# Kernel optimization log

Measured on AMD Instinct MI355X. Metric: run time of the kernel, lower is better.

The kernel has to match this reference:

```python
import jax, jax.numpy as jnp
import numpy as np


def _gcn_conv(x, W, b, src, dst, deg_inv_sqrt, n_nodes):
    # x: [N, Fin], W: [Fin, Fout]; edges (with self-loops): src, dst [E+N]
    h = x @ W  # [N, Fout]
    norm = deg_inv_sqrt[src] * deg_inv_sqrt[dst]  # [E+N]
    msgs = h[src] * norm[:, None]  # gather-multiply
    out = jax.ops.segment_sum(msgs, dst, num_segments=n_nodes)  # scatter-add
    return out + b


def setup_inputs() -> dict:
    key = jax.random.key(0)
    k1, k2, k3, k4 = jax.random.split(key, 4)
    N, E, FIN, HID, OUT = 100000, 3200000, 128, 32, 32
    x = jax.random.normal(k1, (N, FIN), dtype=jnp.float32)
    edge_index = jax.random.randint(k2, (2, E), 0, N, dtype=jnp.int64)
    W1 = jax.random.normal(k3, (FIN, HID), dtype=jnp.float32) * (1.0 / np.sqrt(FIN))
    b1 = jnp.zeros((HID,), dtype=jnp.float32)
    W2 = jax.random.normal(k4, (HID, OUT), dtype=jnp.float32) * (1.0 / np.sqrt(HID))
    b2 = jnp.zeros((OUT,), dtype=jnp.float32)
    return {"x": x, "edge_index": edge_index, "W1": W1, "b1": b1, "W2": W2, "b2": b2}


def reference(x, edge_index, W1, b1, W2, b2):
    n = x.shape[0]
    # GCNConv defaults: add self-loops, symmetric normalization D^-1/2 (A+I) D^-1/2
    loops = jnp.arange(n, dtype=edge_index.dtype)
    src = jnp.concatenate([edge_index[0], loops])
    dst = jnp.concatenate([edge_index[1], loops])
    deg = jax.ops.segment_sum(jnp.ones_like(dst, dtype=x.dtype), dst, num_segments=n)
    deg_inv_sqrt = jnp.where(deg > 0, jax.lax.rsqrt(jnp.maximum(deg, 1.0)), 0.0)
    h = jax.nn.relu(_gcn_conv(x, W1, b1, src, dst, deg_inv_sqrt, n))  # hidden layer + ReLU
    out = jax.nn.relu(_gcn_conv(h, W2, b2, src, dst, deg_inv_sqrt, n))  # last layer + last_activation relu
    return out
```

## Files before the change

### kernel.cpp

```cpp
#include <hip/hip_runtime.h>
#include <hip/hip_fp16.h>

#define FIN 128
#define HID 32
#define BSHIFT 8
#define BNODES 256
#define CHUNK 2048
#define NBMAX 512
#define CAPB 8960
#define G1ROWS 64
#define XPAD 4


__global__ __launch_bounds__(256) void chunk_sort_kernel(const int* __restrict__ src,
                                                         const int* __restrict__ dst,
                                                         int* __restrict__ ec,
                                                         unsigned short* __restrict__ offt,
                                                         int E, int nb) {
    __shared__ int hist[NBMAX];
    __shared__ int pref[NBMAX];
    __shared__ int sorted[CHUNK];
    int c = blockIdx.x, t = threadIdx.x;
    int beg = c * CHUNK;
    int cnt = min(CHUNK, E - beg);
    for (int i = t; i < nb; i += 256) hist[i] = 0;
    __syncthreads();
    int bk[8], ent[8];
    #pragma unroll
    for (int j = 0; j < 8; ++j) {
        int i = t + j * 256;
        if (i < cnt) {
            int d = dst[beg + i];
            bk[j]  = ((unsigned)d) >> BSHIFT;
            ent[j] = src[beg + i] | ((d & (BNODES - 1)) << 24);
            atomicAdd(&hist[bk[j]], 1);
        } else bk[j] = -1;
    }
    __syncthreads();
    if (t < 64) {
        int v[8];
        int s = 0;
        #pragma unroll
        for (int j = 0; j < 8; ++j) {
            int idx = t * 8 + j;
            int h = (idx < nb) ? hist[idx] : 0;
            v[j] = s; s += h;
        }
        int run = s;
        #pragma unroll
        for (int d = 1; d < 64; d <<= 1) {
            int o = __shfl_up(run, d, 64);
            if (t >= d) run += o;
        }
        int excl = run - s;
        #pragma unroll
        for (int j = 0; j < 8; ++j) {
            int idx = t * 8 + j;
            if (idx < nb) { int p = excl + v[j]; pref[idx] = p; hist[idx] = p; }
        }
    }
    __syncthreads();
    #pragma unroll
    for (int j = 0; j < 8; ++j) {
        if (bk[j] >= 0) {
            int p = atomicAdd(&hist[bk[j]], 1);
            sorted[p] = ent[j];
        }
    }
    __syncthreads();
    for (int i = t; i < cnt; i += 256) ec[(size_t)c * CHUNK + i] = sorted[i];
    unsigned short* row = offt + (size_t)c * (nb + 1);
    for (int i = t; i < nb; i += 256) row[i] = (unsigned short)pref[i];
    if (t == 0) row[nb] = (unsigned short)cnt;
}


__global__ __launch_bounds__(1024) void bucket_build_kernel(const int* __restrict__ ec,
                                                            const unsigned short* __restrict__ offt,
                                                            int* __restrict__ entries,
                                                            float* __restrict__ dinv,
                                                            int* __restrict__ rowbeg,
                                                            int* __restrict__ rowcnt,
                                                            int n, int nb, int nchunks, int cap) {
    __shared__ int raw[CAPB];
    __shared__ int srt[CAPB];
    __shared__ int hist[BNODES];
    __shared__ int pref[BNODES];
    __shared__ int cursor[BNODES];
    __shared__ int nfill;
    int b = blockIdx.x, t = threadIdx.x;
    if (t < BNODES) hist[t] = 0;
    if (t == 0) nfill = 0;
    __syncthreads();
    for (int c = t; c < nchunks; c += 1024) {
        const unsigned short* row = offt + (size_t)c * (nb + 1);
        int s = row[b], e2 = row[b + 1];
        int m = e2 - s;
        if (m > 0) {
            int base = atomicAdd(&nfill, m);
            const int* p = ec + (size_t)c * CHUNK + s;
            int k = 0;
            for (; k + 4 <= m; k += 4) {
                int e0 = p[k], e1 = p[k + 1], e2v = p[k + 2], e3 = p[k + 3];
                if (base + k + 0 < CAPB) raw[base + k + 0] = e0;
                if (base + k + 1 < CAPB) raw[base + k + 1] = e1;
                if (base + k + 2 < CAPB) raw[base + k + 2] = e2v;
                if (base + k + 3 < CAPB) raw[base + k + 3] = e3;
                atomicAdd(&hist[((unsigned)e0) >> 24], 1);
                atomicAdd(&hist[((unsigned)e1) >> 24], 1);
                atomicAdd(&hist[((unsigned)e2v) >> 24], 1);
                atomicAdd(&hist[((unsigned)e3) >> 24], 1);
            }
            for (; k < m; ++k) {
                int e = p[k];
                if (base + k < CAPB) raw[base + k] = e;
                atomicAdd(&hist[((unsigned)e) >> 24], 1);
            }
        }
    }
    __syncthreads();
    int total = min(nfill, CAPB);
    if (t < 64) {
        int v[4];
        int s = 0;
        #pragma unroll
        for (int j = 0; j < 4; ++j) { v[j] = s; s += hist[t * 4 + j]; }
        int run = s;
        #pragma unroll
        for (int d = 1; d < 64; d <<= 1) {
            int o = __shfl_up(run, d, 64);
            if (t >= d) run += o;
        }
        int excl = run - s;
        #pragma unroll
        for (int j = 0; j < 4; ++j) {
            int idx = t * 4 + j;
            int p = excl + v[j];
            pref[idx] = p; cursor[idx] = p;
        }
    }
    __syncthreads();
    for (int i = t; i < total; i += 1024) {
        int e = raw[i];
        int p = atomicAdd(&cursor[((unsigned)e) >> 24], 1);
        srt[p] = e;
    }
    __syncthreads();
    int* ep = entries + (size_t)b * cap;
    for (int i = t; i < total; i += 1024) ep[i] = srt[i];
    int node = b * BNODES + t;
    if (t < BNODES && node < n) {
        int deg = hist[t];
        dinv[node]   = rsqrtf((float)deg + 1.0f);
        rowbeg[node] = b * cap + pref[t];
        rowcnt[node] = deg;
    }
}


__global__ __launch_bounds__(256) void gemm1_kernel(const float* __restrict__ x,
                                                    const float* __restrict__ W,
                                                    const float* __restrict__ dinv,
                                                    __half* __restrict__ h16, int n) {
    __shared__ float Ws[FIN * HID];
    int t = threadIdx.x;
    for (int i = t; i < FIN * HID; i += 256) Ws[i] = W[i];
    __syncthreads();
    int row0 = blockIdx.x * G1ROWS;
    int tr = t >> 3, tc = t & 7;
    int r0 = row0 + tr * 2, c0 = tc * 4;
    bool v0 = r0 < n, v1 = (r0 + 1) < n;
    const float* p0 = v0 ? &x[(size_t)r0 * FIN] : x;
    const float* p1 = v1 ? &x[(size_t)(r0 + 1) * FIN] : x;
    float4 a0 = make_float4(0.f, 0.f, 0.f, 0.f);
    float4 a1 = make_float4(0.f, 0.f, 0.f, 0.f);
    #pragma unroll 8
    for (int k4 = 0; k4 < FIN / 4; ++k4) {
        float4 xv0 = *(const float4*)&p0[k4 * 4];
        float4 xv1 = *(const float4*)&p1[k4 * 4];
        float4 w0 = *(const float4*)&Ws[(k4 * 4 + 0) * HID + c0];
        float4 w1 = *(const float4*)&Ws[(k4 * 4 + 1) * HID + c0];
        float4 w2 = *(const float4*)&Ws[(k4 * 4 + 2) * HID + c0];
        float4 w3 = *(const float4*)&Ws[(k4 * 4 + 3) * HID + c0];
        a0.x = fmaf(xv0.x, w0.x, a0.x); a0.y = fmaf(xv0.x, w0.y, a0.y);
        a0.z = fmaf(xv0.x, w0.z, a0.z); a0.w = fmaf(xv0.x, w0.w, a0.w);
        a0.x = fmaf(xv0.y, w1.x, a0.x); a0.y = fmaf(xv0.y, w1.y, a0.y);
        a0.z = fmaf(xv0.y, w1.z, a0.z); a0.w = fmaf(xv0.y, w1.w, a0.w);
        a0.x = fmaf(xv0.z, w2.x, a0.x); a0.y = fmaf(xv0.z, w2.y, a0.y);
        a0.z = fmaf(xv0.z, w2.z, a0.z); a0.w = fmaf(xv0.z, w2.w, a0.w);
        a0.x = fmaf(xv0.w, w3.x, a0.x); a0.y = fmaf(xv0.w, w3.y, a0.y);
        a0.z = fmaf(xv0.w, w3.z, a0.z); a0.w = fmaf(xv0.w, w3.w, a0.w);
        a1.x = fmaf(xv1.x, w0.x, a1.x); a1.y = fmaf(xv1.x, w0.y, a1.y);
        a1.z = fmaf(xv1.x, w0.z, a1.z); a1.w = fmaf(xv1.x, w0.w, a1.w);
        a1.x = fmaf(xv1.y, w1.x, a1.x); a1.y = fmaf(xv1.y, w1.y, a1.y);
        a1.z = fmaf(xv1.y, w1.z, a1.z); a1.w = fmaf(xv1.y, w1.w, a1.w);
        a1.x = fmaf(xv1.z, w2.x, a1.x); a1.y = fmaf(xv1.z, w2.y, a1.y);
        a1.z = fmaf(xv1.z, w2.z, a1.z); a1.w = fmaf(xv1.z, w2.w, a1.w);
        a1.x = fmaf(xv1.w, w3.x, a1.x); a1.y = fmaf(xv1.w, w3.y, a1.y);
        a1.z = fmaf(xv1.w, w3.z, a1.z); a1.w = fmaf(xv1.w, w3.w, a1.w);
    }
    #pragma unroll
    for (int rr = 0; rr < 2; ++rr) {
        int row = r0 + rr;
        float4 a = rr ? a1 : a0;
        float sc = (row < n) ? dinv[row] : 0.f;
        __half2 q0 = __floats2half2_rn(a.x * sc, a.y * sc);
        __half2 q1 = __floats2half2_rn(a.z * sc, a.w * sc);
        __half2* dstp = (__half2*)&h16[(size_t)row * HID + c0];
        dstp[0] = q0;
        dstp[1] = q1;
    }
}


template <int FUSEW2>
__global__ __launch_bounds__(256) void gather_kernel(const int* __restrict__ entries,
                                                     const int* __restrict__ rowbeg,
                                                     const int* __restrict__ rowcnt,
                                                     const float* __restrict__ dinv,
                                                     const __half* __restrict__ h16,
                                                     const float* __restrict__ bias,
                                                     const float* __restrict__ W2,
                                                     __half* __restrict__ houth,
                                                     float* __restrict__ outf,
                                                     int n, int sent) {
    __shared__ float Ws[HID * HID];
    int t = threadIdx.x;
    if (FUSEW2) {
        for (int i = t; i < HID * HID; i += 256) Ws[i] = W2[i];
        __syncthreads();
    }
    int g = t >> 2, f = t & 3;
    int i = blockIdx.x * 64 + g;
    if (i >= n) return;
    float di = dinv[i];
    float a[8];
    {
        float4 sv4 = *(const float4*)&h16[(size_t)i * HID + f * 8];
        const __half2* sh = (const __half2*)&sv4;
        #pragma unroll
        for (int q = 0; q < 4; ++q) {
            float2 fp = __half22float2(sh[q]);
            a[2 * q] = fp.x; a[2 * q + 1] = fp.y;
        }
    }
    int beg = rowbeg[i], cnt = rowcnt[i];
    for (int base = 0; base < cnt; base += 8) {
        int i0 = base + f, i1 = base + 4 + f;
        int sv0 = (i0 < cnt) ? entries[beg + i0] : sent;
        int sv1 = (i1 < cnt) ? entries[beg + i1] : sent;
        sv0 &= 0xFFFFFF; sv1 &= 0xFFFFFF;
        float4 hv[8];
        #pragma unroll
        for (int j = 0; j < 4; ++j) {
            int e = __shfl(sv0, j, 4);
            hv[j] = *(const float4*)&h16[(size_t)e * HID + f * 8];
        }
        #pragma unroll
        for (int j = 0; j < 4; ++j) {
            int e = __shfl(sv1, j, 4);
            hv[4 + j] = *(const float4*)&h16[(size_t)e * HID + f * 8];
        }
        #pragma unroll
        for (int j = 0; j < 8; ++j) {
            const __half2* hp = (const __half2*)&hv[j];
            #pragma unroll
            for (int q = 0; q < 4; ++q) {
                float2 fp = __half22float2(hp[q]);
                a[2 * q] += fp.x; a[2 * q + 1] += fp.y;
            }
        }
    }
    float4 b0 = *(const float4*)&bias[f * 8];
    float4 b1 = *(const float4*)&bias[f * 8 + 4];
    float bj[8] = {b0.x, b0.y, b0.z, b0.w, b1.x, b1.y, b1.z, b1.w};
    float rl[8];
    #pragma unroll
    for (int j = 0; j < 8; ++j) rl[j] = fmaxf(bj[j] + di * a[j], 0.f);

    if (!FUSEW2) {
        *(float4*)&outf[(size_t)i * HID + f * 8]     = make_float4(rl[0], rl[1], rl[2], rl[3]);
        *(float4*)&outf[(size_t)i * HID + f * 8 + 4] = make_float4(rl[4], rl[5], rl[6], rl[7]);
    } else {
        int c0 = f * 8;
        float o[8] = {0.f, 0.f, 0.f, 0.f, 0.f, 0.f, 0.f, 0.f};
        #pragma unroll
        for (int s = 0; s < 4; ++s) {
            #pragma unroll
            for (int j = 0; j < 8; ++j) {
                float av = __shfl(rl[j], s, 4);
                int k = s * 8 + j;
                float4 w0 = *(const float4*)&Ws[k * HID + c0];
                float4 w1 = *(const float4*)&Ws[k * HID + c0 + 4];
                o[0] = fmaf(av, w0.x, o[0]); o[1] = fmaf(av, w0.y, o[1]);
                o[2] = fmaf(av, w0.z, o[2]); o[3] = fmaf(av, w0.w, o[3]);
                o[4] = fmaf(av, w1.x, o[4]); o[5] = fmaf(av, w1.y, o[5]);
                o[6] = fmaf(av, w1.z, o[6]); o[7] = fmaf(av, w1.w, o[7]);
            }
        }
        float4 tmp;
        __half2* hp2 = (__half2*)&tmp;
        #pragma unroll
        for (int j = 0; j < 4; ++j) hp2[j] = __floats2half2_rn(di * o[2 * j], di * o[2 * j + 1]);
        *(float4*)&houth[(size_t)i * HID + f * 8] = tmp;
    }
}

extern "C" void kernel_launch(void* const* d_in, const int* in_sizes, int n_in,
                              void* d_out, int out_size, void* d_ws, size_t ws_size,
                              hipStream_t stream) {
    const float* x  = (const float*)d_in[0];
    const int*   ei = (const int*)d_in[1];
    const float* W1 = (const float*)d_in[2];
    const float* b1 = (const float*)d_in[3];
    const float* W2 = (const float*)d_in[4];
    const float* b2 = (const float*)d_in[5];
    float* out = (float*)d_out;

    int n = in_sizes[0] / FIN;
    int E = in_sizes[1] / 2;
    const int* src = ei;
    const int* dst = ei + E;

    int nb = (n + BNODES - 1) / BNODES;
    int nchunks = (E + CHUNK - 1) / CHUNK;
    int ggrid = (n + G1ROWS) / G1ROWS;
    int npad = ggrid * G1ROWS;
    int cap = CAPB;

    char* ws = (char*)d_ws;
    size_t off = 0;
    auto alloc = [&](size_t bytes) { char* p = ws + off; off += (bytes + 255) & ~(size_t)255; return p; };
    int*            ec      = (int*)alloc((size_t)nchunks * CHUNK * 4);
    unsigned short* offt    = (unsigned short*)alloc((size_t)nchunks * (nb + 1) * 2);
    int*            entries = (int*)alloc((size_t)nb * cap * 4);
    float*          dinv    = (float*)alloc((size_t)n * 4);
    int*            rowbeg  = (int*)alloc((size_t)n * 4);
    int*            rowcnt  = (int*)alloc((size_t)n * 4);
    __half*         hha     = (__half*)alloc((size_t)npad * HID * 2);
    __half*         hhb     = (__half*)alloc((size_t)(n + 1) * HID * 2);

    hipMemsetAsync(hhb + (size_t)n * HID, 0, HID * 2, stream);

    chunk_sort_kernel<<<nchunks, 256, 0, stream>>>(src, dst, ec, offt, E, nb);
    bucket_build_kernel<<<nb, 1024, 0, stream>>>(ec, offt, entries, dinv, rowbeg, rowcnt,
                                                 n, nb, nchunks, cap);

    gemm1_kernel<<<ggrid, 256, 0, stream>>>(x, W1, dinv, hha, n);
    gather_kernel<1><<<(n + 63) / 64, 256, 0, stream>>>(entries, rowbeg, rowcnt, dinv, hha,
                                                        b1, W2, hhb, nullptr, n, n);

    gather_kernel<0><<<(n + 63) / 64, 256, 0, stream>>>(entries, rowbeg, rowcnt, dinv, hhb,
                                                        b2, nullptr, nullptr, out, n, n);
}
```

Measured before the change: 242.6 us.

## Transpose chunk offset table, lane-split bucket copy, drop shared sort buffer

Chunks grow to 4096 edges with 512-thread blocks, and the per-chunk bucket offset table is stored transposed so each bucket's offsets sit contiguously across chunks, making bucket_build's offset reads coalesced. Bucket build now uses 512 threads with four lanes per chunk cooperatively copying entries, which replaces serial per-thread loops. The scatter into sorted order writes straight to global memory instead of staging through a second shared array, cutting shared memory and a sync. The costs are strided scattered writes of the transposed offsets in chunk_sort and uncoalesced global scatter writes in bucket build.

```diff
diff --git a/kernel.cpp b/kernel.cpp
--- a/kernel.cpp
+++ b/kernel.cpp
@@ -5,30 +5,29 @@
 #define HID 32
 #define BSHIFT 8
 #define BNODES 256
-#define CHUNK 2048
+#define CHUNK 4096
 #define NBMAX 512
 #define CAPB 8960
 #define G1ROWS 64
-#define XPAD 4
-
-
-__global__ __launch_bounds__(256) void chunk_sort_kernel(const int* __restrict__ src,
+
+
+__global__ __launch_bounds__(512) void chunk_sort_kernel(const int* __restrict__ src,
                                                          const int* __restrict__ dst,
                                                          int* __restrict__ ec,
-                                                         unsigned short* __restrict__ offt,
-                                                         int E, int nb) {
+                                                         unsigned short* __restrict__ offtT,
+                                                         int E, int nb, int nchunks) {
     __shared__ int hist[NBMAX];
     __shared__ int pref[NBMAX];
     __shared__ int sorted[CHUNK];
     int c = blockIdx.x, t = threadIdx.x;
     int beg = c * CHUNK;
     int cnt = min(CHUNK, E - beg);
-    for (int i = t; i < nb; i += 256) hist[i] = 0;
+    for (int i = t; i < nb; i += 512) hist[i] = 0;
     __syncthreads();
     int bk[8], ent[8];
     #pragma unroll
     for (int j = 0; j < 8; ++j) {
-        int i = t + j * 256;
+        int i = t + j * 512;
         if (i < cnt) {
             int d = dst[beg + i];
             bk[j]  = ((unsigned)d) >> BSHIFT;
@@ -68,22 +67,20 @@
         }
     }
     __syncthreads();
-    for (int i = t; i < cnt; i += 256) ec[(size_t)c * CHUNK + i] = sorted[i];
-    unsigned short* row = offt + (size_t)c * (nb + 1);
-    for (int i = t; i < nb; i += 256) row[i] = (unsigned short)pref[i];
-    if (t == 0) row[nb] = (unsigned short)cnt;
-}
-
-
-__global__ __launch_bounds__(1024) void bucket_build_kernel(const int* __restrict__ ec,
-                                                            const unsigned short* __restrict__ offt,
-                                                            int* __restrict__ entries,
-                                                            float* __restrict__ dinv,
-                                                            int* __restrict__ rowbeg,
-                                                            int* __restrict__ rowcnt,
-                                                            int n, int nb, int nchunks, int cap) {
+    for (int i = t; i < cnt; i += 512) ec[(size_t)c * CHUNK + i] = sorted[i];
+    for (int i = t; i < nb; i += 512) offtT[(size_t)i * nchunks + c] = (unsigned short)pref[i];
+    if (t == 0) offtT[(size_t)nb * nchunks + c] = (unsigned short)cnt;
+}
+
+
+__global__ __launch_bounds__(512) void bucket_build_kernel(const int* __restrict__ ec,
+                                                           const unsigned short* __restrict__ offtT,
+                                                           int* __restrict__ entries,
+                                                           float* __restrict__ dinv,
+                                                           int* __restrict__ rowbeg,
+                                                           int* __restrict__ rowcnt,
+                                                           int n, int nb, int nchunks, int cap) {
     __shared__ int raw[CAPB];
-    __shared__ int srt[CAPB];
     __shared__ int hist[BNODES];
     __shared__ int pref[BNODES];
     __shared__ int cursor[BNODES];
@@ -92,26 +89,18 @@
     if (t < BNODES) hist[t] = 0;
     if (t == 0) nfill = 0;
     __syncthreads();
-    for (int c = t; c < nchunks; c += 1024) {
-        const unsigned short* row = offt + (size_t)c * (nb + 1);
-        int s = row[b], e2 = row[b + 1];
+    const unsigned short* r0 = offtT + (size_t)b * nchunks;
+    const unsigned short* r1 = offtT + (size_t)(b + 1) * nchunks;
+    int lane = t & 3;
+    for (int c = (t >> 2); c < nchunks; c += 128) {
+        int s = r0[c], e2 = r1[c];
         int m = e2 - s;
         if (m > 0) {
-            int base = atomicAdd(&nfill, m);
+            int base;
+            if (lane == 0) base = atomicAdd(&nfill, m);
+            base = __shfl(base, 0, 4);
             const int* p = ec + (size_t)c * CHUNK + s;
-            int k = 0;
-            for (; k + 4 <= m; k += 4) {
-                int e0 = p[k], e1 = p[k + 1], e2v = p[k + 2], e3 = p[k + 3];
-                if (base + k + 0 < CAPB) raw[base + k + 0] = e0;
-                if (base + k + 1 < CAPB) raw[base + k + 1] = e1;
-                if (base + k + 2 < CAPB) raw[base + k + 2] = e2v;
-                if (base + k + 3 < CAPB) raw[base + k + 3] = e3;
-                atomicAdd(&hist[((unsigned)e0) >> 24], 1);
-                atomicAdd(&hist[((unsigned)e1) >> 24], 1);
-                atomicAdd(&hist[((unsigned)e2v) >> 24], 1);
-                atomicAdd(&hist[((unsigned)e3) >> 24], 1);
-            }
-            for (; k < m; ++k) {
+            for (int k = lane; k < m; k += 4) {
                 int e = p[k];
                 if (base + k < CAPB) raw[base + k] = e;
                 atomicAdd(&hist[((unsigned)e) >> 24], 1);
@@ -140,14 +129,12 @@
         }
     }
     __syncthreads();
-    for (int i = t; i < total; i += 1024) {
+    int* ep = entries + (size_t)b * cap;
+    for (int i = t; i < total; i += 512) {
         int e = raw[i];
         int p = atomicAdd(&cursor[((unsigned)e) >> 24], 1);
-        srt[p] = e;
-    }
-    __syncthreads();
-    int* ep = entries + (size_t)b * cap;
-    for (int i = t; i < total; i += 1024) ep[i] = srt[i];
+        ep[p] = e;
+    }
     int node = b * BNODES + t;
     if (t < BNODES && node < n) {
         int deg = hist[t];
@@ -332,7 +319,7 @@
     size_t off = 0;
     auto alloc = [&](size_t bytes) { char* p = ws + off; off += (bytes + 255) & ~(size_t)255; return p; };
     int*            ec      = (int*)alloc((size_t)nchunks * CHUNK * 4);
-    unsigned short* offt    = (unsigned short*)alloc((size_t)nchunks * (nb + 1) * 2);
+    unsigned short* offtT   = (unsigned short*)alloc((size_t)(nb + 1) * nchunks * 2);
     int*            entries = (int*)alloc((size_t)nb * cap * 4);
     float*          dinv    = (float*)alloc((size_t)n * 4);
     int*            rowbeg  = (int*)alloc((size_t)n * 4);
@@ -342,9 +329,9 @@
 
     hipMemsetAsync(hhb + (size_t)n * HID, 0, HID * 2, stream);
 
-    chunk_sort_kernel<<<nchunks, 256, 0, stream>>>(src, dst, ec, offt, E, nb);
-    bucket_build_kernel<<<nb, 1024, 0, stream>>>(ec, offt, entries, dinv, rowbeg, rowcnt,
-                                                 n, nb, nchunks, cap);
+    chunk_sort_kernel<<<nchunks, 512, 0, stream>>>(src, dst, ec, offtT, E, nb, nchunks);
+    bucket_build_kernel<<<nb, 512, 0, stream>>>(ec, offtT, entries, dinv, rowbeg, rowcnt,
+                                                n, nb, nchunks, cap);
 
     gemm1_kernel<<<ggrid, 256, 0, stream>>>(x, W1, dinv, hha, n);
     gather_kernel<1><<<(n + 63) / 64, 256, 0, stream>>>(entries, rowbeg, rowcnt, dinv, hha,
```

After: 248.0 us. 2.2% more time.

## Split neighbor gather into two source-range passes for cache locality

Applied to the files above, without the earlier changes.

Each node's edge list is sorted into two halves by whether the source index falls below or above n/2, and each aggregation runs as two passes, one per source range. A float accumulator carries the partial sum between passes. Each pass then touches only half of the feature table, which should fit better in L2/MALL and cut random-gather misses. The cost is an extra kernel launch per layer, a round trip of an n x 32 float accumulator, and twice the index and rowbeg reads.

```diff
diff --git a/kernel.cpp b/kernel.cpp
--- a/kernel.cpp
+++ b/kernel.cpp
@@ -9,7 +9,6 @@
 #define NBMAX 512
 #define CAPB 8960
 #define G1ROWS 64
-#define XPAD 4
 
 
 __global__ __launch_bounds__(256) void chunk_sort_kernel(const int* __restrict__ src,
@@ -80,16 +79,18 @@
                                                             int* __restrict__ entries,
                                                             float* __restrict__ dinv,
                                                             int* __restrict__ rowbeg,
+                                                            int* __restrict__ rowmid,
                                                             int* __restrict__ rowcnt,
-                                                            int n, int nb, int nchunks, int cap) {
+                                                            int n, int nb, int nchunks, int cap,
+                                                            int half) {
     __shared__ int raw[CAPB];
     __shared__ int srt[CAPB];
-    __shared__ int hist[BNODES];
-    __shared__ int pref[BNODES];
-    __shared__ int cursor[BNODES];
+    __shared__ int hist[2 * BNODES];
+    __shared__ int pref[2 * BNODES];
+    __shared__ int cursor[2 * BNODES];
     __shared__ int nfill;
     int b = blockIdx.x, t = threadIdx.x;
-    if (t < BNODES) hist[t] = 0;
+    for (int i = t; i < 2 * BNODES; i += 1024) hist[i] = 0;
     if (t == 0) nfill = 0;
     __syncthreads();
     for (int c = t; c < nchunks; c += 1024) {
@@ -106,25 +107,25 @@
                 if (base + k + 1 < CAPB) raw[base + k + 1] = e1;
                 if (base + k + 2 < CAPB) raw[base + k + 2] = e2v;
                 if (base + k + 3 < CAPB) raw[base + k + 3] = e3;
-                atomicAdd(&hist[((unsigned)e0) >> 24], 1);
-                atomicAdd(&hist[((unsigned)e1) >> 24], 1);
-                atomicAdd(&hist[((unsigned)e2v) >> 24], 1);
-                atomicAdd(&hist[((unsigned)e3) >> 24], 1);
+                atomicAdd(&hist[((((unsigned)e0) >> 24) << 1) | ((e0 & 0xFFFFFF) >= half)], 1);
+                atomicAdd(&hist[((((unsigned)e1) >> 24) << 1) | ((e1 & 0xFFFFFF) >= half)], 1);
+                atomicAdd(&hist[((((unsigned)e2v) >> 24) << 1) | ((e2v & 0xFFFFFF) >= half)], 1);
+                atomicAdd(&hist[((((unsigned)e3) >> 24) << 1) | ((e3 & 0xFFFFFF) >= half)], 1);
             }
             for (; k < m; ++k) {
                 int e = p[k];
                 if (base + k < CAPB) raw[base + k] = e;
-                atomicAdd(&hist[((unsigned)e) >> 24], 1);
+                atomicAdd(&hist[((((unsigned)e) >> 24) << 1) | ((e & 0xFFFFFF) >= half)], 1);
             }
         }
     }
     __syncthreads();
     int total = min(nfill, CAPB);
     if (t < 64) {
-        int v[4];
+        int v[8];
         int s = 0;
         #pragma unroll
-        for (int j = 0; j < 4; ++j) { v[j] = s; s += hist[t * 4 + j]; }
+        for (int j = 0; j < 8; ++j) { v[j] = s; s += hist[t * 8 + j]; }
         int run = s;
         #pragma unroll
         for (int d = 1; d < 64; d <<= 1) {
@@ -133,8 +134,8 @@
         }
         int excl = run - s;
         #pragma unroll
-        for (int j = 0; j < 4; ++j) {
-            int idx = t * 4 + j;
+        for (int j = 0; j < 8; ++j) {
+            int idx = t * 8 + j;
             int p = excl + v[j];
             pref[idx] = p; cursor[idx] = p;
         }
@@ -142,7 +143,8 @@
     __syncthreads();
     for (int i = t; i < total; i += 1024) {
         int e = raw[i];
-        int p = atomicAdd(&cursor[((unsigned)e) >> 24], 1);
+        int key = ((((unsigned)e) >> 24) << 1) | ((e & 0xFFFFFF) >= half);
+        int p = atomicAdd(&cursor[key], 1);
         srt[p] = e;
     }
     __syncthreads();
@@ -150,9 +152,11 @@
     for (int i = t; i < total; i += 1024) ep[i] = srt[i];
     int node = b * BNODES + t;
     if (t < BNODES && node < n) {
-        int deg = hist[t];
+        int d0 = hist[2 * t], d1 = hist[2 * t + 1];
+        int deg = d0 + d1;
         dinv[node]   = rsqrtf((float)deg + 1.0f);
-        rowbeg[node] = b * cap + pref[t];
+        rowbeg[node] = b * cap + pref[2 * t];
+        rowmid[node] = d0;
         rowcnt[node] = deg;
     }
 }
@@ -213,42 +217,53 @@
 }
 
 
-template <int FUSEW2>
+template <int PASS, int FUSEW2>
 __global__ __launch_bounds__(256) void gather_kernel(const int* __restrict__ entries,
                                                      const int* __restrict__ rowbeg,
+                                                     const int* __restrict__ rowmid,
                                                      const int* __restrict__ rowcnt,
                                                      const float* __restrict__ dinv,
                                                      const __half* __restrict__ h16,
                                                      const float* __restrict__ bias,
                                                      const float* __restrict__ W2,
+                                                     float* __restrict__ acc,
                                                      __half* __restrict__ houth,
                                                      float* __restrict__ outf,
                                                      int n, int sent) {
     __shared__ float Ws[HID * HID];
     int t = threadIdx.x;
-    if (FUSEW2) {
+    if (PASS == 1 && FUSEW2) {
         for (int i = t; i < HID * HID; i += 256) Ws[i] = W2[i];
         __syncthreads();
     }
     int g = t >> 2, f = t & 3;
     int i = blockIdx.x * 64 + g;
     if (i >= n) return;
-    float di = dinv[i];
     float a[8];
-    {
+    int beg = rowbeg[i];
+    int lo, hi;
+    if (PASS == 0) {
+        lo = 0; hi = rowmid[i];
+        #pragma unroll
+        for (int j = 0; j < 8; ++j) a[j] = 0.f;
+    } else {
+        lo = rowmid[i]; hi = rowcnt[i];
+        float4 pa0 = *(const float4*)&acc[(size_t)i * HID + f * 8];
+        float4 pa1 = *(const float4*)&acc[(size_t)i * HID + f * 8 + 4];
+        a[0] = pa0.x; a[1] = pa0.y; a[2] = pa0.z; a[3] = pa0.w;
+        a[4] = pa1.x; a[5] = pa1.y; a[6] = pa1.z; a[7] = pa1.w;
         float4 sv4 = *(const float4*)&h16[(size_t)i * HID + f * 8];
         const __half2* sh = (const __half2*)&sv4;
         #pragma unroll
         for (int q = 0; q < 4; ++q) {
             float2 fp = __half22float2(sh[q]);
-            a[2 * q] = fp.x; a[2 * q + 1] = fp.y;
-        }
-    }
-    int beg = rowbeg[i], cnt = rowcnt[i];
-    for (int base = 0; base < cnt; base += 8) {
+            a[2 * q] += fp.x; a[2 * q + 1] += fp.y;
+        }
+    }
+    for (int base = lo; base < hi; base += 8) {
         int i0 = base + f, i1 = base + 4 + f;
-        int sv0 = (i0 < cnt) ? entries[beg + i0] : sent;
-        int sv1 = (i1 < cnt) ? entries[beg + i1] : sent;
+        int sv0 = (i0 < hi) ? entries[beg + i0] : sent;
+        int sv1 = (i1 < hi) ? entries[beg + i1] : sent;
         sv0 &= 0xFFFFFF; sv1 &= 0xFFFFFF;
         float4 hv[8];
         #pragma unroll
@@ -271,6 +286,12 @@
             }
         }
     }
+    if (PASS == 0) {
+        *(float4*)&acc[(size_t)i * HID + f * 8]     = make_float4(a[0], a[1], a[2], a[3]);
+        *(float4*)&acc[(size_t)i * HID + f * 8 + 4] = make_float4(a[4], a[5], a[6], a[7]);
+        return;
+    }
+    float di = dinv[i];
     float4 b0 = *(const float4*)&bias[f * 8];
     float4 b1 = *(const float4*)&bias[f * 8 + 4];
     float bj[8] = {b0.x, b0.y, b0.z, b0.w, b1.x, b1.y, b1.z, b1.w};
@@ -327,6 +348,7 @@
     int ggrid = (n + G1ROWS) / G1ROWS;
     int npad = ggrid * G1ROWS;
     int cap = CAPB;
+    int half = n / 2;
 
     char* ws = (char*)d_ws;
     size_t off = 0;
@@ -336,20 +358,27 @@
     int*            entries = (int*)alloc((size_t)nb * cap * 4);
     float*          dinv    = (float*)alloc((size_t)n * 4);
     int*            rowbeg  = (int*)alloc((size_t)n * 4);
+    int*            rowmid  = (int*)alloc((size_t)n * 4);
     int*            rowcnt  = (int*)alloc((size_t)n * 4);
+    float*          acc     = (float*)alloc((size_t)n * HID * 4);
     __half*         hha     = (__half*)alloc((size_t)npad * HID * 2);
     __half*         hhb     = (__half*)alloc((size_t)(n + 1) * HID * 2);
 
     hipMemsetAsync(hhb + (size_t)n * HID, 0, HID * 2, stream);
 
     chunk_sort_kernel<<<nchunks, 256, 0, stream>>>(src, dst, ec, offt, E, nb);
-    bucket_build_kernel<<<nb, 1024, 0, stream>>>(ec, offt, entries, dinv, rowbeg, rowcnt,
-                                                 n, nb, nchunks, cap);
-
+    bucket_build_kernel<<<nb, 1024, 0, stream>>>(ec, offt, entries, dinv, rowbeg, rowmid,
+                                                 rowcnt, n, nb, nchunks, cap, half);
+
+    int ggath = (n + 63) / 64;
     gemm1_kernel<<<ggrid, 256, 0, stream>>>(x, W1, dinv, hha, n);
-    gather_kernel<1><<<(n + 63) / 64, 256, 0, stream>>>(entries, rowbeg, rowcnt, dinv, hha,
-                                                        b1, W2, hhb, nullptr, n, n);
-
-    gather_kernel<0><<<(n + 63) / 64, 256, 0, stream>>>(entries, rowbeg, rowcnt, dinv, hhb,
-                                                        b2, nullptr, nullptr, out, n, n);
-}
+    gather_kernel<0, 0><<<ggath, 256, 0, stream>>>(entries, rowbeg, rowmid, rowcnt, dinv, hha,
+                                                   nullptr, nullptr, acc, nullptr, nullptr, n, n);
+    gather_kernel<1, 1><<<ggath, 256, 0, stream>>>(entries, rowbeg, rowmid, rowcnt, dinv, hha,
+                                                   b1, W2, acc, hhb, nullptr, n, n);
+
+    gather_kernel<0, 0><<<ggath, 256, 0, stream>>>(entries, rowbeg, rowmid, rowcnt, dinv, hhb,
+                                                   nullptr, nullptr, acc, nullptr, nullptr, n, n);
+    gather_kernel<1, 0><<<ggath, 256, 0, stream>>>(entries, rowbeg, rowmid, rowcnt, dinv, hhb,
+                                                   b2, nullptr, acc, nullptr, out, n, n);
+}
```

Measured after the change: 245.6 us. Within noise of the previous version (+1.2%).
